# Performance work log

Hardware: AMD Instinct MI355X
Metric: run time of the kernel (lower is better)

Reference implementation:

```python
import jax, jax.numpy as jnp
import numpy as np

EMBED_DIM = 1024
NUM_HEADS = 16
HEAD_DIM = EMBED_DIM // NUM_HEADS


def setup_inputs() -> dict:
    key = jax.random.key(0)
    ks = jax.random.split(key, 5)
    B, S, D = 2, 2048, EMBED_DIM
    scale_w = 1.0 / np.sqrt(D)
    x = jax.random.normal(ks[0], (B, S, D), dtype=jnp.float32)
    Wq = jax.random.normal(ks[1], (D, D), dtype=jnp.float32) * scale_w
    Wk = jax.random.normal(ks[2], (D, D), dtype=jnp.float32) * scale_w
    Wv = jax.random.normal(ks[3], (D, D), dtype=jnp.float32) * scale_w
    Wo = jax.random.normal(ks[4], (D, D), dtype=jnp.float32) * scale_w
    return {"x": x, "Wq": Wq, "Wk": Wk, "Wv": Wv, "Wo": Wo}


def reference(x, Wq, Wk, Wv, Wo):
    B, S, D = x.shape
    H, Dh = NUM_HEADS, HEAD_DIM
    scale = 1.0 / jnp.sqrt(jnp.asarray(Dh, dtype=x.dtype))

    def split_heads(t):
        return t.reshape(B, S, H, Dh).transpose(0, 2, 1, 3)  # [B,H,S,Dh]

    q = split_heads(x @ Wq)
    k = split_heads(x @ Wk)
    v = split_heads(x @ Wv)

    scores = jnp.einsum("bhqd,bhkd->bhqk", q, k) * scale
    causal = jnp.tril(jnp.ones((S, S), dtype=bool))[None, None]
    scores = jnp.where(causal, scores, jnp.asarray(-1e9, dtype=scores.dtype))
    weights = jax.nn.softmax(scores, axis=-1)
    attn = jnp.einsum("bhqk,bhkd->bhqd", weights, v)
    attn = attn.transpose(0, 2, 1, 3).reshape(B, S, D)
    return attn @ Wo
```

## Files before the change

kernel.cpp:

```cpp
#include <hip/hip_runtime.h>
#include <cstdint>

typedef __bf16 bf16;
typedef __bf16 bf16x2 __attribute__((ext_vector_type(2)));
typedef __bf16 bf16x4 __attribute__((ext_vector_type(4)));
typedef __bf16 bf16x8 __attribute__((ext_vector_type(8)));
typedef float f32x4 __attribute__((ext_vector_type(4)));

constexpr int S = 2048, D = 1024, H = 16, HD = 64, B = 2;
constexpr size_t TSZ = (size_t)B * H * S * HD;

__device__ __forceinline__ f32x4 mfma16(bf16x8 a, bf16x8 b, f32x4 c) {
  return __builtin_amdgcn_mfma_f32_16x16x32_bf16(a, b, c, 0, 0, 0);
}

__device__ __forceinline__ void gl_lds16(const bf16* g, bf16* s) {
  __builtin_amdgcn_global_load_lds((__attribute__((address_space(1))) void*)g,
                                   (__attribute__((address_space(3))) void*)s,
                                   16, 0, 0);
}

__global__ __launch_bounds__(256) void prep_all(const float* __restrict__ x,
                                                const float* __restrict__ W0,
                                                const float* __restrict__ W1,
                                                const float* __restrict__ W2,
                                                const float* __restrict__ W3,
                                                bf16* __restrict__ xb,
                                                bf16* __restrict__ Wt) {
  __shared__ __align__(16) bf16 Lt[64][68];
  const int bid = blockIdx.x, t = threadIdx.x;
  if (bid < 2048) {
    const size_t i = (size_t)bid * 256 + t;
    const float4 a = ((const float4*)x)[2 * i];
    const float4 b = ((const float4*)x)[2 * i + 1];
    bf16x8 o = {(bf16)a.x, (bf16)a.y, (bf16)a.z, (bf16)a.w,
                (bf16)b.x, (bf16)b.y, (bf16)b.z, (bf16)b.w};
    *(bf16x8*)&xb[i * 8] = o;
    return;
  }
  const int r = bid - 2048;
  const int z = r >> 8, rest = r & 255;
  const float* W = z == 0 ? W0 : z == 1 ? W1 : z == 2 ? W2 : W3;
  const int k0 = (rest & 15) * 64, n0 = (rest >> 4) * 64;
  const int tr = t >> 4, tc = (t & 15) * 4;
#pragma unroll
  for (int p = 0; p < 4; ++p) {
    const int rr = 16 * p + tr;
    const float4 v = *(const float4*)&W[(size_t)(k0 + rr) * D + n0 + tc];
    Lt[tc + 0][rr] = (bf16)v.x;
    Lt[tc + 1][rr] = (bf16)v.y;
    Lt[tc + 2][rr] = (bf16)v.z;
    Lt[tc + 3][rr] = (bf16)v.w;
  }
  __syncthreads();
#pragma unroll
  for (int p = 0; p < 4; ++p) {
    const int n = 16 * p + tr;
    const bf16x4 o = *(const bf16x4*)&Lt[n][tc];
    *(bf16x4*)&Wt[((size_t)z * D + n0 + n) * D + k0 + tc] = o;
  }
}

template <int MODE, int BNT>
__global__ __launch_bounds__(256) void gemm_bt(const bf16* __restrict__ A,
                                               const bf16* __restrict__ Bt,
                                               void* __restrict__ Cp) {
  constexpr int K = 1024;
  constexpr int NI = BNT / 32;
  __shared__ __align__(16) bf16 As[128 * 64];
  __shared__ __align__(16) bf16 Bs[BNT * 64];

  const int bid = blockIdx.x, nwg = gridDim.x;
  const int lg = (bid & 7) * (nwg >> 3) + (bid >> 3);
  const int bm = (lg & 31) * 128;
  const int bn = (lg >> 5) * BNT;

  const int t = threadIdx.x, l = t & 63, w = t >> 6;
  const int c = l & 15, g = l >> 4, cx = c & 7;
  const int lrow = l >> 3;
  const int srcc = ((l & 7) ^ lrow) << 3;
  const int wm = (w >> 1) * 64, wn = (w & 1) * (BNT / 2);

  f32x4 acc[4][NI] = {};

  for (int kt = 0; kt < K / 64; ++kt) {
    const int k0 = kt * 64;
    __syncthreads();
#pragma unroll
    for (int i = 0; i < 4; ++i) {
      const int ci = i * 4 + w;
      const int row = ci * 8 + lrow;
      gl_lds16(A + (size_t)(bm + row) * K + k0 + srcc, As + ci * 512 + l * 8);
    }
#pragma unroll
    for (int i = 0; i < BNT / 32; ++i) {
      const int ci = i * 4 + w;
      const int row = ci * 8 + lrow;
      gl_lds16(Bt + (size_t)(bn + row) * K + k0 + srcc, Bs + ci * 512 + l * 8);
    }
    __syncthreads();

    bf16x8 af[4][2], bfv[NI][2];
#pragma unroll
    for (int mi = 0; mi < 4; ++mi) {
      const int row = wm + mi * 16 + c;
#pragma unroll
      for (int kh = 0; kh < 2; ++kh)
        af[mi][kh] = *(const bf16x8*)&As[row * 64 + (((kh * 4 + g) ^ cx) << 3)];
    }
#pragma unroll
    for (int ni = 0; ni < NI; ++ni) {
      const int row = wn + ni * 16 + c;
#pragma unroll
      for (int kh = 0; kh < 2; ++kh)
        bfv[ni][kh] = *(const bf16x8*)&Bs[row * 64 + (((kh * 4 + g) ^ cx) << 3)];
    }
#pragma unroll
    for (int mi = 0; mi < 4; ++mi)
#pragma unroll
      for (int ni = 0; ni < NI; ++ni) {
        acc[mi][ni] = mfma16(af[mi][0], bfv[ni][0], acc[mi][ni]);
        acc[mi][ni] = mfma16(af[mi][1], bfv[ni][1], acc[mi][ni]);
      }
  }

#pragma unroll
  for (int mi = 0; mi < 4; ++mi)
#pragma unroll
    for (int ni = 0; ni < NI; ++ni)
#pragma unroll
      for (int r = 0; r < 4; ++r) {
        const int m = bm + wm + mi * 16 + 4 * g + r;
        const int n = bn + wn + ni * 16 + c;
        const float v = acc[mi][ni][r];
        if constexpr (MODE == 0) {
          const int which = n >> 10, nn = n & 1023;
          const int h = nn >> 6, d = nn & 63;
          const int bb = m >> 11, s = m & 2047;
          ((bf16*)Cp)[which * TSZ + ((((size_t)bb * H + h) * S + s) << 6) + d] =
              (bf16)v;
        } else {
          ((float*)Cp)[(size_t)m * D + n] = v;
        }
      }
}

__global__ __launch_bounds__(256, 3) void attn14(const bf16* __restrict__ Q,
                                                 const bf16* __restrict__ Kg,
                                                 const bf16* __restrict__ Vg,
                                                 bf16* __restrict__ Ab,
                                                 bf16* __restrict__ Op,
                                                 float* __restrict__ ML) {
  __shared__ __align__(16) bf16 Ks[2 * 64 * 64];
  __shared__ __align__(16) bf16 Vt[64 * 64];

  const int bid = blockIdx.x;
  const int e = bid >> 5, bh = bid & 31;
  int j, kvA, kvB, half;
  bool split;
  if (e < 16) {
    j = 15 - (e >> 1); half = e & 1; split = true;
    kvA = half * (j + 1); kvB = kvA + (j + 1);
  } else {
    j = e - 16; half = 0; split = false;
    kvA = 0; kvB = 2 * j + 2;
  }

  const int t = threadIdx.x, l = t & 63, w = t >> 6;
  const int c = l & 15, g = l >> 4, cx = c & 7;
  const int bb = bh >> 4, h = bh & 15;
  const float SC = 0.18033688011112042f;
  const float THRS = 44.3614195558365f;

  const bf16* Kbase = Kg + (size_t)bh * S * HD;
  const bf16* Vbase = Vg + (size_t)bh * S * HD;

  const int q0 = j * 128;
  const int qga = q0 + 32 * w + c;
  const int qgb = qga + 16;
  const bf16* Qa = Q + ((size_t)bh * S + qga) * HD;
  const bf16* Qb = Q + ((size_t)bh * S + qgb) * HD;
  const bf16x8 qfa0 = *(const bf16x8*)&Qa[g * 8];
  const bf16x8 qfa1 = *(const bf16x8*)&Qa[32 + g * 8];
  const bf16x8 qfb0 = *(const bf16x8*)&Qb[g * 8];
  const bf16x8 qfb1 = *(const bf16x8*)&Qb[32 + g * 8];

  const int lrow = l >> 3;
  const int srcc = ((l & 7) ^ lrow) << 3;
  const int p2 = t & 31, dgv = t >> 5;
  const int hv = p2 >> 4;
  const int gv = (p2 >> 1) & 3;
  const int jv = ((p2 >> 3) & 1) * 4 + (p2 & 1) * 2;
  const int vchunk = (hv << 2) | gv;

  {
    const bf16* K0 = Kbase + (size_t)kvA * 64 * HD;
    bf16* kd = Ks + (kvA & 1) * 4096;
    gl_lds16(K0 + (size_t)(w * 8 + lrow) * 64 + srcc, kd + w * 512 + l * 8);
    gl_lds16(K0 + (size_t)((4 + w) * 8 + lrow) * 64 + srcc,
             kd + (4 + w) * 512 + l * 8);
  }
  __builtin_amdgcn_sched_barrier(0);
  bf16x8 va0 = *(const bf16x8*)&Vbase[((size_t)kvA * 64 + 2 * p2) * 64 + dgv * 8];
  bf16x8 va1 = *(const bf16x8*)&Vbase[((size_t)kvA * 64 + 2 * p2 + 1) * 64 + dgv * 8];

  f32x4 oacc_a[4] = {}, oacc_b[4] = {};
  float mrun_a = -1e30f, lrun_a = 0.f;
  float mrun_b = -1e30f, lrun_b = 0.f;

  for (int kt = kvA; kt < kvB; ++kt) {
    __builtin_amdgcn_s_barrier();
    __builtin_amdgcn_sched_barrier(0);

    if (kt + 1 < kvB) {
      const bf16* Kn = Kbase + (size_t)(kt + 1) * 64 * HD;
      bf16* kd = Ks + ((kt + 1) & 1) * 4096;
      gl_lds16(Kn + (size_t)(w * 8 + lrow) * 64 + srcc, kd + w * 512 + l * 8);
      gl_lds16(Kn + (size_t)((4 + w) * 8 + lrow) * 64 + srcc,
               kd + (4 + w) * 512 + l * 8);
    }
    __builtin_amdgcn_sched_barrier(0);

#pragma unroll
    for (int i = 0; i < 8; ++i) {
      bf16x2 pr2 = {va0[i], va1[i]};
      *(bf16x2*)&Vt[(8 * dgv + i) * 64 + ((vchunk ^ i) << 3) + jv] = pr2;
    }
    {
      const int ktn = (kt + 1 < kvB) ? kt + 1 : kt;
      const bf16* Vs = Vbase + (size_t)ktn * 64 * HD;
      va0 = *(const bf16x8*)&Vs[(2 * p2) * 64 + dgv * 8];
      va1 = *(const bf16x8*)&Vs[(2 * p2 + 1) * 64 + dgv * 8];
    }
    asm volatile("s_waitcnt lgkmcnt(0)" ::: "memory");
    __builtin_amdgcn_s_barrier();
    __builtin_amdgcn_sched_barrier(0);

    const bf16* kbuf = Ks + (kt & 1) * 4096;

    f32x4 st_a[4], st_b[4];
    __builtin_amdgcn_s_setprio(1);
#pragma unroll
    for (int ct = 0; ct < 4; ++ct) {
      const int krow = ct * 16 + c;
      const bf16x8 kf0 = *(const bf16x8*)&kbuf[krow * 64 + ((g ^ cx) << 3)];
      const bf16x8 kf1 = *(const bf16x8*)&kbuf[krow * 64 + (((4 + g) ^ cx) << 3)];
      f32x4 za = {}, zb = {};
      za = mfma16(kf0, qfa0, za);
      st_a[ct] = mfma16(kf1, qfa1, za);
      zb = mfma16(kf0, qfb0, zb);
      st_b[ct] = mfma16(kf1, qfb1, zb);
    }
    __builtin_amdgcn_s_setprio(0);

    if (64 * kt + 63 > q0 + 32 * w) {
#pragma unroll
      for (int ct = 0; ct < 4; ++ct)
#pragma unroll
        for (int r = 0; r < 4; ++r) {
          const int kv = kt * 64 + ct * 16 + 4 * g + r;
          if (kv > qga) st_a[ct][r] = -1e30f;
          if (kv > qgb) st_b[ct][r] = -1e30f;
        }
    }

    {
      float tm[4];
#pragma unroll
      for (int ct = 0; ct < 4; ++ct)
        tm[ct] = fmaxf(fmaxf(st_a[ct][0], st_a[ct][1]),
                       fmaxf(st_a[ct][2], st_a[ct][3]));
      float mt = fmaxf(fmaxf(tm[0], tm[1]), fmaxf(tm[2], tm[3]));
      mt = fmaxf(mt, __shfl_xor(mt, 16));
      mt = fmaxf(mt, __shfl_xor(mt, 32));
      if (!__all(mt <= mrun_a + THRS)) {
        const float mnew = fmaxf(mrun_a, mt);
        const float fac = __builtin_amdgcn_exp2f((mrun_a - mnew) * SC);
        lrun_a *= fac;
#pragma unroll
        for (int ct = 0; ct < 4; ++ct)
#pragma unroll
          for (int r = 0; r < 4; ++r) oacc_a[ct][r] *= fac;
        mrun_a = mnew;
      }
    }
    {
      float tm[4];
#pragma unroll
      for (int ct = 0; ct < 4; ++ct)
        tm[ct] = fmaxf(fmaxf(st_b[ct][0], st_b[ct][1]),
                       fmaxf(st_b[ct][2], st_b[ct][3]));
      float mt = fmaxf(fmaxf(tm[0], tm[1]), fmaxf(tm[2], tm[3]));
      mt = fmaxf(mt, __shfl_xor(mt, 16));
      mt = fmaxf(mt, __shfl_xor(mt, 32));
      if (!__all(mt <= mrun_b + THRS)) {
        const float mnew = fmaxf(mrun_b, mt);
        const float fac = __builtin_amdgcn_exp2f((mrun_b - mnew) * SC);
        lrun_b *= fac;
#pragma unroll
        for (int ct = 0; ct < 4; ++ct)
#pragma unroll
          for (int r = 0; r < 4; ++r) oacc_b[ct][r] *= fac;
        mrun_b = mnew;
      }
    }
    float pa[4][4], pb[4][4];
    float sqa[4], sqb[4];
#pragma unroll
    for (int ct = 0; ct < 4; ++ct) {
#pragma unroll
      for (int r = 0; r < 4; ++r) {
        pa[ct][r] = __builtin_amdgcn_exp2f((st_a[ct][r] - mrun_a) * SC);
        pb[ct][r] = __builtin_amdgcn_exp2f((st_b[ct][r] - mrun_b) * SC);
      }
      sqa[ct] = (pa[ct][0] + pa[ct][1]) + (pa[ct][2] + pa[ct][3]);
      sqb[ct] = (pb[ct][0] + pb[ct][1]) + (pb[ct][2] + pb[ct][3]);
    }
    lrun_a += (sqa[0] + sqa[1]) + (sqa[2] + sqa[3]);
    lrun_b += (sqb[0] + sqb[1]) + (sqb[2] + sqb[3]);

    const bf16x8 pa0_a = {(bf16)pa[0][0], (bf16)pa[0][1], (bf16)pa[0][2], (bf16)pa[0][3],
                          (bf16)pa[1][0], (bf16)pa[1][1], (bf16)pa[1][2], (bf16)pa[1][3]};
    const bf16x8 pa1_a = {(bf16)pa[2][0], (bf16)pa[2][1], (bf16)pa[2][2], (bf16)pa[2][3],
                          (bf16)pa[3][0], (bf16)pa[3][1], (bf16)pa[3][2], (bf16)pa[3][3]};
    const bf16x8 pa0_b = {(bf16)pb[0][0], (bf16)pb[0][1], (bf16)pb[0][2], (bf16)pb[0][3],
                          (bf16)pb[1][0], (bf16)pb[1][1], (bf16)pb[1][2], (bf16)pb[1][3]};
    const bf16x8 pa1_b = {(bf16)pb[2][0], (bf16)pb[2][1], (bf16)pb[2][2], (bf16)pb[2][3],
                          (bf16)pb[3][0], (bf16)pb[3][1], (bf16)pb[3][2], (bf16)pb[3][3]};

    __builtin_amdgcn_s_setprio(1);
#pragma unroll
    for (int ct = 0; ct < 4; ++ct) {
      const int vrow = ct * 16 + c;
      const bf16x8 vt0 = *(const bf16x8*)&Vt[vrow * 64 + ((g ^ cx) << 3)];
      const bf16x8 vt1 = *(const bf16x8*)&Vt[vrow * 64 + (((4 + g) ^ cx) << 3)];
      oacc_a[ct] = mfma16(vt0, pa0_a, oacc_a[ct]);
      oacc_a[ct] = mfma16(vt1, pa1_a, oacc_a[ct]);
      oacc_b[ct] = mfma16(vt0, pa0_b, oacc_b[ct]);
      oacc_b[ct] = mfma16(vt1, pa1_b, oacc_b[ct]);
    }
    __builtin_amdgcn_s_setprio(0);
  }

  float lt_a = lrun_a, lt_b = lrun_b;
  lt_a += __shfl_xor(lt_a, 16); lt_a += __shfl_xor(lt_a, 32);
  lt_b += __shfl_xor(lt_b, 16); lt_b += __shfl_xor(lt_b, 32);
  const float inva = 1.f / lt_a, invb = 1.f / lt_b;

  if (!split) {
    bf16* Oa = Ab + ((size_t)bb * S + qga) * D + h * 64;
    bf16* Ob = Ab + ((size_t)bb * S + qgb) * D + h * 64;
#pragma unroll
    for (int ct = 0; ct < 4; ++ct)
#pragma unroll
      for (int pr = 0; pr < 2; ++pr) {
        bf16x2 ka = {(bf16)(oacc_a[ct][2 * pr] * inva),
                     (bf16)(oacc_a[ct][2 * pr + 1] * inva)};
        bf16x2 kb = {(bf16)(oacc_b[ct][2 * pr] * invb),
                     (bf16)(oacc_b[ct][2 * pr + 1] * invb)};
        *(bf16x2*)&Oa[ct * 16 + 4 * g + 2 * pr] = ka;
        *(bf16x2*)&Ob[ct * 16 + 4 * g + 2 * pr] = kb;
      }
  } else {
    const size_t ra = ((size_t)bh * 1024 + (qga - 1024)) * 2 + half;
    const size_t rb = ((size_t)bh * 1024 + (qgb - 1024)) * 2 + half;
    bf16* Pa = Op + ra * 64;
    bf16* Pb = Op + rb * 64;
#pragma unroll
    for (int ct = 0; ct < 4; ++ct)
#pragma unroll
      for (int pr = 0; pr < 2; ++pr) {
        bf16x2 ka = {(bf16)(oacc_a[ct][2 * pr] * inva),
                     (bf16)(oacc_a[ct][2 * pr + 1] * inva)};
        bf16x2 kb = {(bf16)(oacc_b[ct][2 * pr] * invb),
                     (bf16)(oacc_b[ct][2 * pr + 1] * invb)};
        *(bf16x2*)&Pa[ct * 16 + 4 * g + 2 * pr] = ka;
        *(bf16x2*)&Pb[ct * 16 + 4 * g + 2 * pr] = kb;
      }
    if (g == 0) {
      ML[ra * 2] = mrun_a; ML[ra * 2 + 1] = lt_a;
      ML[rb * 2] = mrun_b; ML[rb * 2 + 1] = lt_b;
    }
  }
}

__global__ __launch_bounds__(256) void attn_merge2(const bf16* __restrict__ Op,
                                                   const float* __restrict__ ML,
                                                   bf16* __restrict__ Ab) {
  const float SC = 0.18033688011112042f;
  const int rid = blockIdx.x * 4 + (threadIdx.x >> 6);
  const int lane = threadIdx.x & 63;
  const int bh = rid >> 10, rw = rid & 1023;
  const size_t r2 = (size_t)rid * 2;
  const float m0 = ML[(r2 + 0) * 2], l0 = ML[(r2 + 0) * 2 + 1];
  const float m1 = ML[(r2 + 1) * 2], l1 = ML[(r2 + 1) * 2 + 1];
  const float o0 = (float)Op[(r2 + 0) * 64 + lane];
  const float o1 = (float)Op[(r2 + 1) * 64 + lane];
  const float mn = fmaxf(m0, m1);
  const float w0 = l0 * exp2f((m0 - mn) * SC);
  const float w1 = l1 * exp2f((m1 - mn) * SC);
  const float o = (o0 * w0 + o1 * w1) / (w0 + w1);
  const int bb = bh >> 4, h = bh & 15, s = 1024 + rw;
  Ab[((size_t)bb * S + s) * D + h * 64 + lane] = (bf16)o;
}

extern "C" void kernel_launch(void* const* d_in, const int* in_sizes, int n_in,
                              void* d_out, int out_size, void* d_ws, size_t ws_size,
                              hipStream_t stream) {
  const float* x  = (const float*)d_in[0];
  const float* Wq = (const float*)d_in[1];
  const float* Wk = (const float*)d_in[2];
  const float* Wv = (const float*)d_in[3];
  const float* Wo = (const float*)d_in[4];
  float* out = (float*)d_out;

  bf16* xb  = (bf16*)d_ws;
  bf16* Wt  = xb + (size_t)B * S * D;
  bf16* QKV = Wt + (size_t)4 * D * D;
  bf16* Ab  = QKV + 3 * TSZ;
  bf16* Op  = Ab + TSZ;
  float* ML = (float*)(Op + (size_t)32 * 1024 * 2 * 64);

  prep_all<<<3072, 256, 0, stream>>>(x, Wq, Wk, Wv, Wo, xb, Wt);
  gemm_bt<0, 128><<<768, 256, 0, stream>>>(xb, Wt, QKV);
  attn14<<<768, 256, 0, stream>>>(QKV, QKV + TSZ, QKV + 2 * TSZ, Ab, Op, ML);
  attn_merge2<<<8192, 256, 0, stream>>>(Op, ML, Ab);
  gemm_bt<1, 64><<<512, 256, 0, stream>>>(Ab, Wt + (size_t)3 * D * D, out);
}
```

Measured before the change: 102.4 us.

## Halve attention block to 64 query rows with rebalanced causal split schedule

The attention kernel now runs 128-thread blocks, each covering a 64-row query tile, and the grid doubles to 1536 blocks. The block-to-work mapping is rewritten: the 16 longest query tiles are split in two halves along the KV range and the rest run unsplit. Each thread now loads twice as many K chunks and V rows per tile to make up for the smaller block. The aim is finer-grained load balance and more resident blocks. In exchange, each K/V tile loaded into LDS is shared by fewer queries, so total global traffic rises.

```diff
diff --git a/kernel.cpp b/kernel.cpp
--- a/kernel.cpp
+++ b/kernel.cpp
@@ -145,7 +145,7 @@
       }
 }
 
-__global__ __launch_bounds__(256, 3) void attn14(const bf16* __restrict__ Q,
+__global__ __launch_bounds__(128, 3) void attn15(const bf16* __restrict__ Q,
                                                  const bf16* __restrict__ Kg,
                                                  const bf16* __restrict__ Vg,
                                                  bf16* __restrict__ Ab,
@@ -156,15 +156,11 @@
 
   const int bid = blockIdx.x;
   const int e = bid >> 5, bh = bid & 31;
-  int j, kvA, kvB, half;
+  int qt, kvA, kvB, half;
   bool split;
-  if (e < 16) {
-    j = 15 - (e >> 1); half = e & 1; split = true;
-    kvA = half * (j + 1); kvB = kvA + (j + 1);
-  } else {
-    j = e - 16; half = 0; split = false;
-    kvA = 0; kvB = 2 * j + 2;
-  }
+  if (e < 16)      { qt = 31 - e; half = 0; split = true;  kvA = 0; kvB = (qt + 2) >> 1; }
+  else if (e < 32) { qt = 47 - e; half = 1; split = true;  kvA = (qt + 2) >> 1; kvB = qt + 1; }
+  else             { qt = 47 - e; half = 0; split = false; kvA = 0; kvB = qt + 1; }
 
   const int t = threadIdx.x, l = t & 63, w = t >> 6;
   const int c = l & 15, g = l >> 4, cx = c & 7;
@@ -175,7 +171,7 @@
   const bf16* Kbase = Kg + (size_t)bh * S * HD;
   const bf16* Vbase = Vg + (size_t)bh * S * HD;
 
-  const int q0 = j * 128;
+  const int q0 = qt * 64;
   const int qga = q0 + 32 * w + c;
   const int qgb = qga + 16;
   const bf16* Qa = Q + ((size_t)bh * S + qga) * HD;
@@ -187,7 +183,7 @@
 
   const int lrow = l >> 3;
   const int srcc = ((l & 7) ^ lrow) << 3;
-  const int p2 = t & 31, dgv = t >> 5;
+  const int p2 = t & 31, dgvb = t >> 5;
   const int hv = p2 >> 4;
   const int gv = (p2 >> 1) & 3;
   const int jv = ((p2 >> 3) & 1) * 4 + (p2 & 1) * 2;
@@ -196,13 +192,18 @@
   {
     const bf16* K0 = Kbase + (size_t)kvA * 64 * HD;
     bf16* kd = Ks + (kvA & 1) * 4096;
-    gl_lds16(K0 + (size_t)(w * 8 + lrow) * 64 + srcc, kd + w * 512 + l * 8);
-    gl_lds16(K0 + (size_t)((4 + w) * 8 + lrow) * 64 + srcc,
-             kd + (4 + w) * 512 + l * 8);
+#pragma unroll
+    for (int i = 0; i < 4; ++i) {
+      const int ci = w * 4 + i;
+      gl_lds16(K0 + (size_t)(ci * 8 + lrow) * 64 + srcc, kd + ci * 512 + l * 8);
+    }
   }
   __builtin_amdgcn_sched_barrier(0);
-  bf16x8 va0 = *(const bf16x8*)&Vbase[((size_t)kvA * 64 + 2 * p2) * 64 + dgv * 8];
-  bf16x8 va1 = *(const bf16x8*)&Vbase[((size_t)kvA * 64 + 2 * p2 + 1) * 64 + dgv * 8];
+  const bf16* V0 = Vbase + (size_t)kvA * 64 * HD;
+  bf16x8 va0 = *(const bf16x8*)&V0[(2 * p2) * 64 + dgvb * 8];
+  bf16x8 va1 = *(const bf16x8*)&V0[(2 * p2 + 1) * 64 + dgvb * 8];
+  bf16x8 va2 = *(const bf16x8*)&V0[(2 * p2) * 64 + (dgvb + 4) * 8];
+  bf16x8 va3 = *(const bf16x8*)&V0[(2 * p2 + 1) * 64 + (dgvb + 4) * 8];
 
   f32x4 oacc_a[4] = {}, oacc_b[4] = {};
   float mrun_a = -1e30f, lrun_a = 0.f;
@@ -215,22 +216,28 @@
     if (kt + 1 < kvB) {
       const bf16* Kn = Kbase + (size_t)(kt + 1) * 64 * HD;
       bf16* kd = Ks + ((kt + 1) & 1) * 4096;
-      gl_lds16(Kn + (size_t)(w * 8 + lrow) * 64 + srcc, kd + w * 512 + l * 8);
-      gl_lds16(Kn + (size_t)((4 + w) * 8 + lrow) * 64 + srcc,
-               kd + (4 + w) * 512 + l * 8);
+#pragma unroll
+      for (int i = 0; i < 4; ++i) {
+        const int ci = w * 4 + i;
+        gl_lds16(Kn + (size_t)(ci * 8 + lrow) * 64 + srcc, kd + ci * 512 + l * 8);
+      }
     }
     __builtin_amdgcn_sched_barrier(0);
 
 #pragma unroll
     for (int i = 0; i < 8; ++i) {
-      bf16x2 pr2 = {va0[i], va1[i]};
-      *(bf16x2*)&Vt[(8 * dgv + i) * 64 + ((vchunk ^ i) << 3) + jv] = pr2;
+      bf16x2 w0 = {va0[i], va1[i]};
+      bf16x2 w1 = {va2[i], va3[i]};
+      *(bf16x2*)&Vt[(8 * dgvb + i) * 64 + ((vchunk ^ i) << 3) + jv] = w0;
+      *(bf16x2*)&Vt[(8 * (dgvb + 4) + i) * 64 + ((vchunk ^ i) << 3) + jv] = w1;
     }
     {
       const int ktn = (kt + 1 < kvB) ? kt + 1 : kt;
       const bf16* Vs = Vbase + (size_t)ktn * 64 * HD;
-      va0 = *(const bf16x8*)&Vs[(2 * p2) * 64 + dgv * 8];
-      va1 = *(const bf16x8*)&Vs[(2 * p2 + 1) * 64 + dgv * 8];
+      va0 = *(const bf16x8*)&Vs[(2 * p2) * 64 + dgvb * 8];
+      va1 = *(const bf16x8*)&Vs[(2 * p2 + 1) * 64 + dgvb * 8];
+      va2 = *(const bf16x8*)&Vs[(2 * p2) * 64 + (dgvb + 4) * 8];
+      va3 = *(const bf16x8*)&Vs[(2 * p2 + 1) * 64 + (dgvb + 4) * 8];
     }
     asm volatile("s_waitcnt lgkmcnt(0)" ::: "memory");
     __builtin_amdgcn_s_barrier();
@@ -423,7 +430,7 @@
 
   prep_all<<<3072, 256, 0, stream>>>(x, Wq, Wk, Wv, Wo, xb, Wt);
   gemm_bt<0, 128><<<768, 256, 0, stream>>>(xb, Wt, QKV);
-  attn14<<<768, 256, 0, stream>>>(QKV, QKV + TSZ, QKV + 2 * TSZ, Ab, Op, ML);
+  attn15<<<1536, 128, 0, stream>>>(QKV, QKV + TSZ, QKV + 2 * TSZ, Ab, Op, ML);
   attn_merge2<<<8192, 256, 0, stream>>>(Op, ML, Ab);
   gemm_bt<1, 64><<<512, 256, 0, stream>>>(Ab, Wt + (size_t)3 * D * D, out);
 }
```

After: 106.7 us. +4.2%, slower.
